# Optimization experiments

Measured on AMD Instinct MI355X. Metric: run time of the kernel, lower is better.

Reference implementation:

```python
import jax, jax.numpy as jnp
import numpy as np

B, N, H, NH = 4, 2048, 1024, 16
HD = H // NH  # head_dim = 64


def setup_inputs() -> dict:
    key = jax.random.key(0)
    k1, k2, k3 = jax.random.split(key, 3)
    s = 1.0 / np.sqrt(H)
    return {
        "x": jax.random.normal(k1, (B, N, H), dtype=jnp.float32),
        "w_qkv": jax.random.normal(k2, (3 * H, H), dtype=jnp.float32) * s,
        "b_qkv": jnp.zeros((3 * H,), dtype=jnp.float32),
        "w_out": jax.random.normal(k3, (H, H), dtype=jnp.float32) * s,
        "b_out": jnp.zeros((H,), dtype=jnp.float32),
    }


def reference(x, w_qkv, b_qkv, w_out, b_out):
    b, n, h = x.shape
    qkv = x @ w_qkv.T + b_qkv  # [b, n, 3h]
    q, k, v = jnp.split(qkv, 3, axis=-1)
    # [b, n, h] -> [b, nh, n, hd]
    def heads(t):
        return t.reshape(b, n, NH, HD).transpose(0, 2, 1, 3)
    q, k, v = heads(q), heads(k), heads(v)
    scale = HD ** -0.5
    dots = jnp.einsum('bhqd,bhkd->bhqk', q, k) * scale
    attn = jax.nn.softmax(dots, axis=-1)
    out = jnp.einsum('bhqk,bhkd->bhqd', attn, v)
    out = out.transpose(0, 2, 1, 3).reshape(b, n, h)
    return out @ w_out.T + b_out
```

## Files before the change

### kernel.cpp

```cpp
#include <hip/hip_runtime.h>

typedef __bf16 bf16x8 __attribute__((ext_vector_type(8)));
typedef float f32x4 __attribute__((ext_vector_type(4)));
typedef float f32x16 __attribute__((ext_vector_type(16)));
typedef unsigned int uint2v __attribute__((ext_vector_type(2)));

#define LOG2E 1.44269504088896340736f

#if __has_builtin(__builtin_amdgcn_exp2f)
#define EXP2(x) __builtin_amdgcn_exp2f(x)
#else
#define EXP2(x) exp2f(x)
#endif

static __device__ __forceinline__ unsigned short f2bf(float f) {
    unsigned int u = __builtin_bit_cast(unsigned int, f);
    u += 0x7fffu + ((u >> 16) & 1u);
    return (unsigned short)(u >> 16);
}

static __device__ __forceinline__ void plswap(unsigned int& a, unsigned int& b) {
#if __has_builtin(__builtin_amdgcn_permlane32_swap)
    uint2v r = __builtin_amdgcn_permlane32_swap(a, b, false, false);
    a = r.x; b = r.y;
#else
    asm("v_permlane32_swap_b32 %0, %1" : "+v"(a), "+v"(b));
#endif
}

static __device__ __forceinline__ float xhalf_add(float x) {
    unsigned int a = __builtin_bit_cast(unsigned int, x), b = a;
    plswap(a, b);
    return __builtin_bit_cast(float, a) + __builtin_bit_cast(float, b);
}

__global__ void cvt_kernel(const float* __restrict__ in, unsigned short* __restrict__ out, int n4) {
    int i = blockIdx.x * blockDim.x + threadIdx.x;
    int stride = gridDim.x * blockDim.x;
    for (; i < n4; i += stride) {
        float4 v = reinterpret_cast<const float4*>(in)[i];
        ushort4 o;
        o.x = f2bf(v.x); o.y = f2bf(v.y); o.z = f2bf(v.z); o.w = f2bf(v.w);
        reinterpret_cast<ushort4*>(out)[i] = o;
    }
}

template <int MODE>
__global__ __launch_bounds__(256, 2) void gemm_bt(const unsigned short* __restrict__ A,
                                                  const unsigned short* __restrict__ B,
                                                  const float* __restrict__ bias,
                                                  void* __restrict__ Cout,
                                                  int M, int N, int K) {
    __shared__ unsigned short As[2][128 * 64];
    __shared__ unsigned short Bs[2][128 * 64];
    const int tid = threadIdx.x;
    const int w = tid >> 6, lane = tid & 63;
    const int wr = w >> 1, wc = w & 1;
    const int bm0 = blockIdx.y << 7, bn0 = blockIdx.x << 7;
    const int l15 = lane & 15, l4 = lane >> 4;

    const int srow = w * 8 + (lane >> 3);
    const int gch = (lane & 7) ^ (lane >> 3);

    f32x4 acc[4][4] = {};

    auto stage = [&](int buf, int kt) {
        const int k0 = kt << 6;
        #pragma unroll
        for (int i = 0; i < 4; ++i) {
            int row = i * 32 + srow;
            const unsigned short* ga = A + (size_t)(bm0 + row) * K + k0 + gch * 8;
            __builtin_amdgcn_global_load_lds(
                (const __attribute__((address_space(1))) void*)ga,
                (__attribute__((address_space(3))) void*)&As[buf][i * 2048 + w * 512],
                16, 0, 0);
            const unsigned short* gb = B + (size_t)(bn0 + row) * K + k0 + gch * 8;
            __builtin_amdgcn_global_load_lds(
                (const __attribute__((address_space(1))) void*)gb,
                (__attribute__((address_space(3))) void*)&Bs[buf][i * 2048 + w * 512],
                16, 0, 0);
        }
    };

    const int nk = K >> 6;
    stage(0, 0);
    __syncthreads();
    int buf = 0;
    for (int kt = 0; kt < nk; ++kt) {
        if (kt + 1 < nk) stage(buf ^ 1, kt + 1);
        const unsigned short* as = &As[buf][0];
        const unsigned short* bs = &Bs[buf][0];
        #pragma unroll
        for (int s = 0; s < 2; ++s) {
            bf16x8 af[4], bfr[4];
            #pragma unroll
            for (int t = 0; t < 4; ++t) {
                int rowa = wr * 64 + t * 16 + l15;
                int cha = (s * 4 + l4) ^ (rowa & 7);
                af[t] = *(const bf16x8*)&as[rowa * 64 + cha * 8];
                int rowb = wc * 64 + t * 16 + l15;
                int chb = (s * 4 + l4) ^ (rowb & 7);
                bfr[t] = *(const bf16x8*)&bs[rowb * 64 + chb * 8];
            }
            #pragma unroll
            for (int i = 0; i < 4; ++i)
                #pragma unroll
                for (int j = 0; j < 4; ++j)
                    acc[i][j] = __builtin_amdgcn_mfma_f32_16x16x32_bf16(af[i], bfr[j], acc[i][j], 0, 0, 0);
        }
        __syncthreads();
        buf ^= 1;
    }

    if (MODE == 0) {
        unsigned short* O = (unsigned short*)Cout;
        #pragma unroll
        for (int j = 0; j < 4; ++j) {
            int col = bn0 + wc * 64 + j * 16 + l15;
            float bv = bias[col];
            int which = col >> 10;
            int h = (col >> 6) & 15;
            int d = col & 63;
            #pragma unroll
            for (int i = 0; i < 4; ++i) {
                #pragma unroll
                for (int r = 0; r < 4; ++r) {
                    int row = bm0 + wr * 64 + i * 16 + l4 * 4 + r;
                    int b = row >> 11, n = row & 2047;
                    float v = acc[i][j][r] + bv;
                    size_t idx;
                    if (which == 0) { v *= 0.125f * LOG2E; idx = ((size_t)((b * 16 + h) * 2048 + n)) * 64 + d; }
                    else if (which == 1) { idx = (size_t)8388608 + ((size_t)((b * 16 + h) * 2048 + n)) * 64 + d; }
                    else { idx = (size_t)16777216 + ((size_t)((b * 16 + h) * 64 + d)) * 2048 + n; }
                    O[idx] = f2bf(v);
                }
            }
        }
    } else {
        float* C = (float*)Cout;
        #pragma unroll
        for (int j = 0; j < 4; ++j) {
            int col = bn0 + wc * 64 + j * 16 + l15;
            float bv = bias[col];
            #pragma unroll
            for (int i = 0; i < 4; ++i) {
                #pragma unroll
                for (int r = 0; r < 4; ++r) {
                    int row = bm0 + wr * 64 + i * 16 + l4 * 4 + r;
                    C[(size_t)row * N + col] = acc[i][j][r] + bv;
                }
            }
        }
    }
}

__global__ __launch_bounds__(256, 2) void attn_kernel(const unsigned short* __restrict__ qkv,
                                                      unsigned short* __restrict__ out) {
    __shared__ unsigned short Klds[2][4096];
    __shared__ unsigned short Vlds[2][4096];

    const int tid = threadIdx.x;
    const int w = tid >> 6, lane = tid & 63;
    const int ql = lane & 31;
    const int hi = lane >> 5;
    const int id = blockIdx.x;
    const int bh = id & 63;
    const int qt = id >> 6;
    const size_t SEC = 8388608;

    const unsigned short* Q  = qkv + (size_t)bh * (2048 * 64);
    const unsigned short* Kp = qkv + SEC + (size_t)bh * (2048 * 64);
    const unsigned short* Vt = qkv + 2 * SEC + (size_t)bh * (64 * 2048);

    const int q0 = qt * 256 + w * 64;

    bf16x8 qbA[4], qbB[4];
    #pragma unroll
    for (int c = 0; c < 4; ++c) {
        qbA[c] = *(const bf16x8*)&Q[(size_t)(q0 + ql) * 64 + c * 16 + hi * 8];
        qbB[c] = *(const bf16x8*)&Q[(size_t)(q0 + 32 + ql) * 64 + c * 16 + hi * 8];
    }

    f32x16 oA0 = {}, oA1 = {}, oB0 = {}, oB1 = {};
    float lsA = 0.f, lsB = 0.f;

    const int sri = lane >> 3;
    const int sch = lane & 7;

    auto stage = [&](int buf, int tile) {
        const int kb = tile * 64;
        #pragma unroll
        for (int i = 0; i < 2; ++i) {
            const int r = w * 16 + i * 8 + sri;
            const int c = sch ^ (r & 7);
            const unsigned short* gk = Kp + (size_t)(kb + r) * 64 + c * 8;
            __builtin_amdgcn_global_load_lds(
                (const __attribute__((address_space(1))) void*)gk,
                (__attribute__((address_space(3))) void*)&Klds[buf][w * 1024 + i * 512],
                16, 0, 0);
            const unsigned short* gv = Vt + (size_t)r * 2048 + kb + c * 8;
            __builtin_amdgcn_global_load_lds(
                (const __attribute__((address_space(1))) void*)gv,
                (__attribute__((address_space(3))) void*)&Vlds[buf][w * 1024 + i * 512],
                16, 0, 0);
        }
    };

    auto softmax_block = [&](f32x16& s0, f32x16& s1, float& lsum,
                             bf16x8 (&p0)[2], bf16x8 (&p1)[2]) {
        #pragma unroll
        for (int r = 0; r < 16; ++r) s0[r] = EXP2(s0[r]);
        #pragma unroll
        for (int r = 0; r < 16; ++r) s1[r] = EXP2(s1[r]);
        float u0 = ((s0[0] + s0[1]) + (s0[2] + s0[3])) + ((s0[4] + s0[5]) + (s0[6] + s0[7]));
        float u1 = ((s0[8] + s0[9]) + (s0[10] + s0[11])) + ((s0[12] + s0[13]) + (s0[14] + s0[15]));
        float u2 = ((s1[0] + s1[1]) + (s1[2] + s1[3])) + ((s1[4] + s1[5]) + (s1[6] + s1[7]));
        float u3 = ((s1[8] + s1[9]) + (s1[10] + s1[11])) + ((s1[12] + s1[13]) + (s1[14] + s1[15]));
        float rs = (u0 + u1) + (u2 + u3);
        lsum += xhalf_add(rs);
        #pragma unroll
        for (int g = 0; g < 2; ++g) {
            unsigned int x0, x1, x2, x3;
            asm("v_cvt_pk_bf16_f32 %0, %1, %2" : "=v"(x0) : "v"(s0[8*g + 0]), "v"(s0[8*g + 1]));
            asm("v_cvt_pk_bf16_f32 %0, %1, %2" : "=v"(x1) : "v"(s0[8*g + 2]), "v"(s0[8*g + 3]));
            asm("v_cvt_pk_bf16_f32 %0, %1, %2" : "=v"(x2) : "v"(s0[8*g + 4]), "v"(s0[8*g + 5]));
            asm("v_cvt_pk_bf16_f32 %0, %1, %2" : "=v"(x3) : "v"(s0[8*g + 6]), "v"(s0[8*g + 7]));
            plswap(x0, x2);
            plswap(x1, x3);
            uint4 wds; wds.x = x0; wds.y = x1; wds.z = x2; wds.w = x3;
            p0[g] = __builtin_bit_cast(bf16x8, wds);
        }
        #pragma unroll
        for (int g = 0; g < 2; ++g) {
            unsigned int x0, x1, x2, x3;
            asm("v_cvt_pk_bf16_f32 %0, %1, %2" : "=v"(x0) : "v"(s1[8*g + 0]), "v"(s1[8*g + 1]));
            asm("v_cvt_pk_bf16_f32 %0, %1, %2" : "=v"(x1) : "v"(s1[8*g + 2]), "v"(s1[8*g + 3]));
            asm("v_cvt_pk_bf16_f32 %0, %1, %2" : "=v"(x2) : "v"(s1[8*g + 4]), "v"(s1[8*g + 5]));
            asm("v_cvt_pk_bf16_f32 %0, %1, %2" : "=v"(x3) : "v"(s1[8*g + 6]), "v"(s1[8*g + 7]));
            plswap(x0, x2);
            plswap(x1, x3);
            uint4 wds; wds.x = x0; wds.y = x1; wds.z = x2; wds.w = x3;
            p1[g] = __builtin_bit_cast(bf16x8, wds);
        }
    };

    stage(0, 0);
    __syncthreads();

    for (int t = 0; t < 32; ++t) {
        const int cur = t & 1;
        if (t + 1 < 32) stage(cur ^ 1, t + 1);

        bf16x8 k0[4], k1[4];
        #pragma unroll
        for (int mf = 0; mf < 4; ++mf) {
            int c0 = ((mf * 2 + hi) ^ (ql & 7));
            k0[mf] = *(const bf16x8*)&Klds[cur][ql * 64 + c0 * 8];
            k1[mf] = *(const bf16x8*)&Klds[cur][(32 + ql) * 64 + c0 * 8];
        }

        f32x16 sA0 = {}, sA1 = {};
        #pragma unroll
        for (int mf = 0; mf < 4; ++mf)
            sA0 = __builtin_amdgcn_mfma_f32_32x32x16_bf16(k0[mf], qbA[mf], sA0, 0, 0, 0);
        #pragma unroll
        for (int mf = 0; mf < 4; ++mf)
            sA1 = __builtin_amdgcn_mfma_f32_32x32x16_bf16(k1[mf], qbA[mf], sA1, 0, 0, 0);
        f32x16 sB0 = {}, sB1 = {};
        #pragma unroll
        for (int mf = 0; mf < 4; ++mf)
            sB0 = __builtin_amdgcn_mfma_f32_32x32x16_bf16(k0[mf], qbB[mf], sB0, 0, 0, 0);
        #pragma unroll
        for (int mf = 0; mf < 4; ++mf)
            sB1 = __builtin_amdgcn_mfma_f32_32x32x16_bf16(k1[mf], qbB[mf], sB1, 0, 0, 0);

        bf16x8 v0[4], v1[4];
        #pragma unroll
        for (int ks = 0; ks < 4; ++ks) {
            int c0 = ((ks * 2 + hi) ^ (ql & 7));
            v0[ks] = *(const bf16x8*)&Vlds[cur][ql * 64 + c0 * 8];
            v1[ks] = *(const bf16x8*)&Vlds[cur][(32 + ql) * 64 + c0 * 8];
        }

        bf16x8 pA0[2], pA1[2], pB0[2], pB1[2];
        softmax_block(sA0, sA1, lsA, pA0, pA1);
        softmax_block(sB0, sB1, lsB, pB0, pB1);

        oA0 = __builtin_amdgcn_mfma_f32_32x32x16_bf16(v0[0], pA0[0], oA0, 0, 0, 0);
        oA0 = __builtin_amdgcn_mfma_f32_32x32x16_bf16(v0[1], pA0[1], oA0, 0, 0, 0);
        oA0 = __builtin_amdgcn_mfma_f32_32x32x16_bf16(v0[2], pA1[0], oA0, 0, 0, 0);
        oA0 = __builtin_amdgcn_mfma_f32_32x32x16_bf16(v0[3], pA1[1], oA0, 0, 0, 0);
        oA1 = __builtin_amdgcn_mfma_f32_32x32x16_bf16(v1[0], pA0[0], oA1, 0, 0, 0);
        oA1 = __builtin_amdgcn_mfma_f32_32x32x16_bf16(v1[1], pA0[1], oA1, 0, 0, 0);
        oA1 = __builtin_amdgcn_mfma_f32_32x32x16_bf16(v1[2], pA1[0], oA1, 0, 0, 0);
        oA1 = __builtin_amdgcn_mfma_f32_32x32x16_bf16(v1[3], pA1[1], oA1, 0, 0, 0);
        oB0 = __builtin_amdgcn_mfma_f32_32x32x16_bf16(v0[0], pB0[0], oB0, 0, 0, 0);
        oB0 = __builtin_amdgcn_mfma_f32_32x32x16_bf16(v0[1], pB0[1], oB0, 0, 0, 0);
        oB0 = __builtin_amdgcn_mfma_f32_32x32x16_bf16(v0[2], pB1[0], oB0, 0, 0, 0);
        oB0 = __builtin_amdgcn_mfma_f32_32x32x16_bf16(v0[3], pB1[1], oB0, 0, 0, 0);
        oB1 = __builtin_amdgcn_mfma_f32_32x32x16_bf16(v1[0], pB0[0], oB1, 0, 0, 0);
        oB1 = __builtin_amdgcn_mfma_f32_32x32x16_bf16(v1[1], pB0[1], oB1, 0, 0, 0);
        oB1 = __builtin_amdgcn_mfma_f32_32x32x16_bf16(v1[2], pB1[0], oB1, 0, 0, 0);
        oB1 = __builtin_amdgcn_mfma_f32_32x32x16_bf16(v1[3], pB1[1], oB1, 0, 0, 0);

        __syncthreads();
    }

    const int b = bh >> 4, h = bh & 15;
    {
        const float inv = 1.0f / lsA;
        const int n = q0 + ql;
        unsigned short* obase = out + ((size_t)(b * 2048 + n)) * 1024 + h * 64;
        #pragma unroll
        for (int g = 0; g < 4; ++g) {
            int d0 = 8 * g + 4 * hi;
            ushort4 w0, w1;
            w0.x = f2bf(oA0[4 * g + 0] * inv);
            w0.y = f2bf(oA0[4 * g + 1] * inv);
            w0.z = f2bf(oA0[4 * g + 2] * inv);
            w0.w = f2bf(oA0[4 * g + 3] * inv);
            *(ushort4*)(obase + d0) = w0;
            w1.x = f2bf(oA1[4 * g + 0] * inv);
            w1.y = f2bf(oA1[4 * g + 1] * inv);
            w1.z = f2bf(oA1[4 * g + 2] * inv);
            w1.w = f2bf(oA1[4 * g + 3] * inv);
            *(ushort4*)(obase + 32 + d0) = w1;
        }
    }
    {
        const float inv = 1.0f / lsB;
        const int n = q0 + 32 + ql;
        unsigned short* obase = out + ((size_t)(b * 2048 + n)) * 1024 + h * 64;
        #pragma unroll
        for (int g = 0; g < 4; ++g) {
            int d0 = 8 * g + 4 * hi;
            ushort4 w0, w1;
            w0.x = f2bf(oB0[4 * g + 0] * inv);
            w0.y = f2bf(oB0[4 * g + 1] * inv);
            w0.z = f2bf(oB0[4 * g + 2] * inv);
            w0.w = f2bf(oB0[4 * g + 3] * inv);
            *(ushort4*)(obase + d0) = w0;
            w1.x = f2bf(oB1[4 * g + 0] * inv);
            w1.y = f2bf(oB1[4 * g + 1] * inv);
            w1.z = f2bf(oB1[4 * g + 2] * inv);
            w1.w = f2bf(oB1[4 * g + 3] * inv);
            *(ushort4*)(obase + 32 + d0) = w1;
        }
    }
}

extern "C" void kernel_launch(void* const* d_in, const int* in_sizes, int n_in,
                              void* d_out, int out_size, void* d_ws, size_t ws_size,
                              hipStream_t stream) {
    (void)in_sizes; (void)n_in; (void)out_size; (void)ws_size;
    const float* x     = (const float*)d_in[0];
    const float* w_qkv = (const float*)d_in[1];
    const float* b_qkv = (const float*)d_in[2];
    const float* w_out = (const float*)d_in[3];
    const float* b_out = (const float*)d_in[4];

    unsigned short* ws = (unsigned short*)d_ws;
    unsigned short* xb    = ws;
    unsigned short* wqkvb = ws + 8388608;
    unsigned short* woutb = ws + 11534336;
    unsigned short* qkvb  = ws + 12582912;

    cvt_kernel<<<dim3(2048), dim3(256), 0, stream>>>(x, xb, 8388608 / 4);
    cvt_kernel<<<dim3(1024), dim3(256), 0, stream>>>(w_qkv, wqkvb, 3145728 / 4);
    cvt_kernel<<<dim3(512),  dim3(256), 0, stream>>>(w_out, woutb, 1048576 / 4);

    gemm_bt<0><<<dim3(24, 64), dim3(256), 0, stream>>>(xb, wqkvb, b_qkv, (void*)qkvb, 8192, 3072, 1024);

    attn_kernel<<<dim3(512), dim3(256), 0, stream>>>(qkvb, xb);

    gemm_bt<1><<<dim3(8, 64), dim3(256), 0, stream>>>(xb, woutb, b_out, d_out, 8192, 1024, 1024);
}
```

Baseline: 203.0 us.

## Restructure GEMMs into 512-thread 256x128 tiles with interleaved staging and swizzled grid

Replaces the 128x128, 256-thread GEMM with a 256xBN tile run by 8 waves, so each wave computes 128x32 outputs and more data is reused per LDS load. Staging of the next K tile is split into four quarters interleaved with the MFMA groups, with setprio raised around the MFMA bursts. A 1D block index is remapped so consecutive blocks land on different XCDs. The larger tile halves the block count (256 blocks for the output projection), which may under-fill the GPU, and it raises LDS and register pressure.

```diff
diff --git a/kernel.cpp b/kernel.cpp
--- a/kernel.cpp
+++ b/kernel.cpp
@@ -45,89 +45,111 @@
     }
 }
 
-template <int MODE>
-__global__ __launch_bounds__(256, 2) void gemm_bt(const unsigned short* __restrict__ A,
-                                                  const unsigned short* __restrict__ B,
-                                                  const float* __restrict__ bias,
-                                                  void* __restrict__ Cout,
-                                                  int M, int N, int K) {
-    __shared__ unsigned short As[2][128 * 64];
-    __shared__ unsigned short Bs[2][128 * 64];
+template <int BN, int MODE>
+__global__ __launch_bounds__(512, 2) void gemm8(const unsigned short* __restrict__ A,
+                                                const unsigned short* __restrict__ B,
+                                                const float* __restrict__ bias,
+                                                void* __restrict__ Cout,
+                                                int M, int N, int K, int nbx) {
+    constexpr int NG_B = BN / 64;
+    constexpr int NREP = BN / 64;
+    constexpr int NJH = (NREP + 1) / 2;
+    __shared__ unsigned short As[2][256 * 64];
+    __shared__ unsigned short Bs[2][BN * 64];
+
     const int tid = threadIdx.x;
     const int w = tid >> 6, lane = tid & 63;
-    const int wr = w >> 1, wc = w & 1;
-    const int bm0 = blockIdx.y << 7, bn0 = blockIdx.x << 7;
+    const int wr = w >> 2, wc = w & 3;
     const int l15 = lane & 15, l4 = lane >> 4;
 
-    const int srow = w * 8 + (lane >> 3);
-    const int gch = (lane & 7) ^ (lane >> 3);
-
-    f32x4 acc[4][4] = {};
-
-    auto stage = [&](int buf, int kt) {
+    const int cpx = gridDim.x >> 3;
+    const int swz = (blockIdx.x & 7) * cpx + (blockIdx.x >> 3);
+    const int bx = swz % nbx, by = swz / nbx;
+    const int bm0 = by * 256, bn0 = bx * BN;
+
+    const int srow = tid >> 3;
+    const int scs = (tid & 7) ^ (srow & 7);
+    const unsigned short* gA = A + (size_t)(bm0 + srow) * K + scs * 8;
+    const unsigned short* gB = B + (size_t)(bn0 + srow) * K + scs * 8;
+    const int ldsoff = w * 512;
+
+    f32x4 acc[8][NREP] = {};
+
+    auto stg = [&](int buf, int kt, int q) {
         const int k0 = kt << 6;
-        #pragma unroll
-        for (int i = 0; i < 4; ++i) {
-            int row = i * 32 + srow;
-            const unsigned short* ga = A + (size_t)(bm0 + row) * K + k0 + gch * 8;
+        __builtin_amdgcn_global_load_lds(
+            (const __attribute__((address_space(1))) void*)(gA + (size_t)(q * 64) * K + k0),
+            (__attribute__((address_space(3))) void*)&As[buf][q * 4096 + ldsoff],
+            16, 0, 0);
+        if (q < NG_B) {
             __builtin_amdgcn_global_load_lds(
-                (const __attribute__((address_space(1))) void*)ga,
-                (__attribute__((address_space(3))) void*)&As[buf][i * 2048 + w * 512],
+                (const __attribute__((address_space(1))) void*)(gB + (size_t)(q * 64) * K + k0),
+                (__attribute__((address_space(3))) void*)&Bs[buf][q * 4096 + ldsoff],
                 16, 0, 0);
-            const unsigned short* gb = B + (size_t)(bn0 + row) * K + k0 + gch * 8;
-            __builtin_amdgcn_global_load_lds(
-                (const __attribute__((address_space(1))) void*)gb,
-                (__attribute__((address_space(3))) void*)&Bs[buf][i * 2048 + w * 512],
-                16, 0, 0);
         }
     };
 
+    #pragma unroll
+    for (int q = 0; q < 4; ++q) stg(0, 0, q);
+    __syncthreads();
+
     const int nk = K >> 6;
-    stage(0, 0);
-    __syncthreads();
-    int buf = 0;
+    const int rA = wr * 128 + l15;
+    const int rB = wc * (BN / 4) + l15;
+    const int cxor = l15 & 7;
+
     for (int kt = 0; kt < nk; ++kt) {
-        if (kt + 1 < nk) stage(buf ^ 1, kt + 1);
-        const unsigned short* as = &As[buf][0];
-        const unsigned short* bs = &Bs[buf][0];
-        #pragma unroll
-        for (int s = 0; s < 2; ++s) {
-            bf16x8 af[4], bfr[4];
-            #pragma unroll
-            for (int t = 0; t < 4; ++t) {
-                int rowa = wr * 64 + t * 16 + l15;
-                int cha = (s * 4 + l4) ^ (rowa & 7);
-                af[t] = *(const bf16x8*)&as[rowa * 64 + cha * 8];
-                int rowb = wc * 64 + t * 16 + l15;
-                int chb = (s * 4 + l4) ^ (rowb & 7);
-                bfr[t] = *(const bf16x8*)&bs[rowb * 64 + chb * 8];
-            }
-            #pragma unroll
-            for (int i = 0; i < 4; ++i)
-                #pragma unroll
-                for (int j = 0; j < 4; ++j)
-                    acc[i][j] = __builtin_amdgcn_mfma_f32_16x16x32_bf16(af[i], bfr[j], acc[i][j], 0, 0, 0);
-        }
-        __syncthreads();
-        buf ^= 1;
+        const int p = kt & 1;
+        const unsigned short* as = &As[p][0];
+        const unsigned short* bs = &Bs[p][0];
+        const bool pre = (kt + 1 < nk);
+        #pragma unroll
+        for (int q = 0; q < 4; ++q) {
+            if (pre) stg(p ^ 1, kt + 1, q);
+            const int qm = q >> 1, qn = q & 1;
+            bf16x8 af[4][2], bfr[NJH][2];
+            #pragma unroll
+            for (int i2 = 0; i2 < 4; ++i2)
+                #pragma unroll
+                for (int s = 0; s < 2; ++s)
+                    af[i2][s] = *(const bf16x8*)&as[(rA + (qm * 4 + i2) * 16) * 64 + (((s * 4 + l4) ^ cxor)) * 8];
+            #pragma unroll
+            for (int j2 = 0; j2 < NJH; ++j2)
+                #pragma unroll
+                for (int s = 0; s < 2; ++s)
+                    bfr[j2][s] = *(const bf16x8*)&bs[(rB + (qn * NJH + j2) * 16) * 64 + (((s * 4 + l4) ^ cxor)) * 8];
+            __builtin_amdgcn_s_setprio(1);
+            #pragma unroll
+            for (int i2 = 0; i2 < 4; ++i2)
+                #pragma unroll
+                for (int j2 = 0; j2 < NJH; ++j2) {
+                    acc[qm * 4 + i2][qn * NJH + j2] =
+                        __builtin_amdgcn_mfma_f32_16x16x32_bf16(af[i2][0], bfr[j2][0], acc[qm * 4 + i2][qn * NJH + j2], 0, 0, 0);
+                    acc[qm * 4 + i2][qn * NJH + j2] =
+                        __builtin_amdgcn_mfma_f32_16x16x32_bf16(af[i2][1], bfr[j2][1], acc[qm * 4 + i2][qn * NJH + j2], 0, 0, 0);
+                }
+            __builtin_amdgcn_s_setprio(0);
+            __builtin_amdgcn_sched_barrier(0);
+        }
+        if (pre) __syncthreads();
     }
 
     if (MODE == 0) {
         unsigned short* O = (unsigned short*)Cout;
         #pragma unroll
-        for (int j = 0; j < 4; ++j) {
-            int col = bn0 + wc * 64 + j * 16 + l15;
+        for (int nj = 0; nj < NREP; ++nj) {
+            int col = bn0 + wc * (BN / 4) + nj * 16 + l15;
             float bv = bias[col];
             int which = col >> 10;
             int h = (col >> 6) & 15;
             int d = col & 63;
             #pragma unroll
-            for (int i = 0; i < 4; ++i) {
+            for (int mi = 0; mi < 8; ++mi) {
                 #pragma unroll
                 for (int r = 0; r < 4; ++r) {
-                    int row = bm0 + wr * 64 + i * 16 + l4 * 4 + r;
+                    int row = bm0 + wr * 128 + mi * 16 + l4 * 4 + r;
                     int b = row >> 11, n = row & 2047;
-                    float v = acc[i][j][r] + bv;
+                    float v = acc[mi][nj][r] + bv;
                     size_t idx;
                     if (which == 0) { v *= 0.125f * LOG2E; idx = ((size_t)((b * 16 + h) * 2048 + n)) * 64 + d; }
                     else if (which == 1) { idx = (size_t)8388608 + ((size_t)((b * 16 + h) * 2048 + n)) * 64 + d; }
@@ -139,15 +161,15 @@
     } else {
         float* C = (float*)Cout;
         #pragma unroll
-        for (int j = 0; j < 4; ++j) {
-            int col = bn0 + wc * 64 + j * 16 + l15;
+        for (int nj = 0; nj < NREP; ++nj) {
+            int col = bn0 + wc * (BN / 4) + nj * 16 + l15;
             float bv = bias[col];
             #pragma unroll
-            for (int i = 0; i < 4; ++i) {
+            for (int mi = 0; mi < 8; ++mi) {
                 #pragma unroll
                 for (int r = 0; r < 4; ++r) {
-                    int row = bm0 + wr * 64 + i * 16 + l4 * 4 + r;
-                    C[(size_t)row * N + col] = acc[i][j][r] + bv;
+                    int row = bm0 + wr * 128 + mi * 16 + l4 * 4 + r;
+                    C[(size_t)row * N + col] = acc[mi][nj][r] + bv;
                 }
             }
         }
@@ -369,9 +391,9 @@
     cvt_kernel<<<dim3(1024), dim3(256), 0, stream>>>(w_qkv, wqkvb, 3145728 / 4);
     cvt_kernel<<<dim3(512),  dim3(256), 0, stream>>>(w_out, woutb, 1048576 / 4);
 
-    gemm_bt<0><<<dim3(24, 64), dim3(256), 0, stream>>>(xb, wqkvb, b_qkv, (void*)qkvb, 8192, 3072, 1024);
+    gemm8<128, 0><<<dim3(768), dim3(512), 0, stream>>>(xb, wqkvb, b_qkv, (void*)qkvb, 8192, 3072, 1024, 24);
 
     attn_kernel<<<dim3(512), dim3(256), 0, stream>>>(qkvb, xb);
 
-    gemm_bt<1><<<dim3(8, 64), dim3(256), 0, stream>>>(xb, woutb, b_out, d_out, 8192, 1024, 1024);
-}
+    gemm8<128, 1><<<dim3(256), dim3(512), 0, stream>>>(xb, woutb, b_out, d_out, 8192, 1024, 1024, 8);
+}
```

Result: slower. 247.3 us (+21.8%).
